# Performance work log

Measured on AMD Instinct MI355X. Metric: run time of the kernel, lower is better.

The kernel has to match this reference:

```python
import jax, jax.numpy as jnp
import numpy as np


def _patch_desc(x, patch_size):
    # x: (n, c, h, w). Replicate-pad by patch_size//2 and gather all
    # patch_size*patch_size shifted views -> (n, c*p*p, h*w) descriptors.
    n, c, h, w = x.shape
    step = patch_size // 2
    y = jnp.pad(x, ((0, 0), (0, 0), (step, step), (step, step)), mode='edge')
    feats = [y[:, :, i:i + h, j:j + w]
             for i in range(patch_size) for j in range(patch_size)]
    d = jnp.stack(feats, axis=2)            # (n, c, p*p, h, w)
    return d.reshape(n, c * patch_size * patch_size, h * w)


def setup_inputs() -> dict:
    key = jax.random.key(0)
    k1, k2 = jax.random.split(key)
    n, c, h, w = 4, 16, 64, 64
    s = jax.random.normal(k1, (n, c, h, w), dtype=jnp.float32)
    t = jax.random.normal(k2, (n, c, h, w), dtype=jnp.float32)
    return {"s": s, "t": t, "patch_size": 3}


def reference(s, t, patch_size):
    n, c, h, w = s.shape
    q = _patch_desc(s, patch_size)          # (n, d, hw) source queries
    p = _patch_desc(t, patch_size)          # (n, d, hw) target points
    # Squared-L2 nearest neighbor per source patch (exact version of FLANN kNN)
    qn = jnp.sum(q * q, axis=1)             # (n, hw)
    pn = jnp.sum(p * p, axis=1)             # (n, hw)
    cross = jnp.einsum('ndi,ndj->nij', q, p)  # (n, hw_q, hw_t)
    d2 = qn[:, :, None] - 2.0 * cross + pn[:, None, :]
    idx = jnp.argmin(d2, axis=2)            # (n, hw) flat target index
    nnd = jnp.min(d2, axis=2)               # (n, hw) squared distance
    idy = idx // w
    idx_x = idx % w
    nnf = jnp.stack([idy.reshape(n, h, w), idx_x.reshape(n, h, w)], axis=1)
    nnd = nnd.reshape(n, 1, h, w)
    return nnf.astype(jnp.int32), nnd
```

## Files before the change

### kernel.cpp

```cpp
#include <hip/hip_runtime.h>


#define N_  4
#define C_  16
#define H_  64
#define W_  64
#define HW_ 4096
#define K_  160
#define SPLITS_M 4
#define KKSTRIDE 528

#define SPLITS_V 4
#define TILES_PER_SPLIT_V 4

typedef _Float16 f16;
typedef _Float16 f16x8 __attribute__((ext_vector_type(8)));
typedef float    f32x4 __attribute__((ext_vector_type(4)));

__device__ __forceinline__ int iclamp(int v, int lo, int hi) {
    return v < lo ? lo : (v > hi ? hi : v);
}

__device__ __forceinline__ void async_ld16(const void* g, void* l) {
    __builtin_amdgcn_global_load_lds(
        (const __attribute__((address_space(1))) unsigned int*)g,
        (__attribute__((address_space(3))) unsigned int*)l, 16, 0, 0);
}

__global__ __launch_bounds__(256)
void build_desc_norms_kernel(const float* __restrict__ s,
                             const float* __restrict__ t,
                             f16* __restrict__ Qh, f16* __restrict__ Ql,
                             f16* __restrict__ Ph, f16* __restrict__ Pl,
                             float* __restrict__ pn,
                             float* __restrict__ qn) {
    const int y0  = blockIdx.x;
    const int n   = blockIdx.y;
    const int src = blockIdx.z;
    const float* img = (src ? s : t) + n * (C_ * HW_);
    f16* Dh = src ? Qh : Ph;
    f16* Dl = src ? Ql : Pl;
    float* nrm = src ? qn : pn;

    __shared__ float imgS[3][C_][W_];
    __shared__ float nS[4][W_];
    const int tid = threadIdx.x;
    #pragma unroll
    for (int k = 0; k < 12; ++k) {
        const int idx = tid + k * 256;
        const int x = idx & 63, c = (idx >> 6) & 15, r = idx >> 10;
        const int gy = iclamp(y0 + r - 1, 0, H_ - 1);
        imgS[r][c][x] = img[c * HW_ + gy * W_ + x];
    }
    __syncthreads();

    const int q = tid >> 6, x = tid & 63;
    const int pix = y0 * W_ + x;
    float nacc = 0.f;
    #pragma unroll
    for (int u = 0; u < 5; ++u) {
        const int kk = q * 5 + u;
        f16x8 hv, lv;
        if (kk < 18) {
            const int d  = kk >> 1;
            const int c0 = (kk & 1) * 8;
            const int dy = (d * 11) >> 5;
            const int dx = d - dy * 3;
            const int xs = iclamp(x + dx - 1, 0, W_ - 1);
            #pragma unroll
            for (int cc = 0; cc < 8; ++cc) {
                const float v = imgS[dy][c0 + cc][xs];
                const f16 h = (f16)v;
                hv[cc] = h;
                lv[cc] = (f16)(v - (float)h);
                nacc += v * v;
            }
        } else {
            #pragma unroll
            for (int cc = 0; cc < 8; ++cc) { hv[cc] = (f16)0.f; lv[cc] = (f16)0.f; }
        }
        const size_t off = ((size_t)(n * 20 + kk) * HW_ + pix) * 8;
        *(f16x8*)&Dh[off] = hv;
        *(f16x8*)&Dl[off] = lv;
    }
    nS[q][x] = nacc;
    __syncthreads();
    if (tid < W_)
        nrm[n * HW_ + pix] = nS[0][tid] + nS[1][tid] + nS[2][tid] + nS[3][tid];
}

__global__ __launch_bounds__(256)
void mfma_nn_kernel(const f16* __restrict__ Qh, const f16* __restrict__ Ql,
                    const f16* __restrict__ Ph, const f16* __restrict__ Pl,
                    const float* __restrict__ pn_g,
                    unsigned long long* __restrict__ partial) {
    const int bid   = blockIdx.x;
    const int split = bid & 3;
    const int n     = (bid >> 2) & 3;
    const int iblk  = bid >> 4;
    const int tid  = threadIdx.x;
    const int wave = tid >> 6, lane = tid & 63;
    const int m = lane & 15, quad = lane >> 4;
    const int irow0 = iblk * 128 + wave * 32;

    __shared__ f16 B0[20 * KKSTRIDE];
    __shared__ f16 B1[20 * KKSTRIDE];
    __shared__ f16 B2[20 * KKSTRIDE];
    __shared__ float pnS[1024];

    f16x8 Ah[2][5], Al[2][5];
    #pragma unroll
    for (int is = 0; is < 2; ++is)
        #pragma unroll
        for (int kc = 0; kc < 5; ++kc) {
            const size_t off = ((size_t)(n * 20 + kc * 4 + quad) * HW_ +
                                irow0 + is * 16 + m) * 8;
            Ah[is][kc] = *(const f16x8*)(Qh + off);
            Al[is][kc] = *(const f16x8*)(Ql + off);
        }

    const int jsplit0 = split * 1024;
    #pragma unroll
    for (int k = 0; k < 4; ++k)
        pnS[tid + k * 256] = pn_g[n * HW_ + jsplit0 + tid + k * 256];

    float    bd[2][4];
    unsigned bj[2][4];
    #pragma unroll
    for (int is = 0; is < 2; ++is)
        #pragma unroll
        for (int rg = 0; rg < 4; ++rg) { bd[is][rg] = 3.0e38f; bj[is][rg] = 0u; }

    const int skk  = wave * 5;
    const int sarr = lane >> 5;
    const int srow = lane & 31;
    const f16* sbase = sarr ? Pl : Ph;

    #define STAGE(BUF, T)                                                     \
        {   _Pragma("unroll")                                                 \
            for (int u = 0; u < 5; ++u) {                                     \
                const int kk = skk + u;                                       \
                const f16* g = sbase + ((size_t)(n * 20 + kk) * HW_ +         \
                                        jsplit0 + (T) * 32 + srow) * 8;       \
                async_ld16(g, (void*)&BUF[kk * KKSTRIDE + lane * 8]);         \
            }                                                                 \
        }

    #define COMPUTE(BUF, T)                                                   \
        {   _Pragma("unroll")                                                 \
            for (int js = 0; js < 2; ++js) {                                  \
                f32x4 Cf[2];                                                  \
                Cf[0] = (f32x4){0.f, 0.f, 0.f, 0.f};                          \
                Cf[1] = (f32x4){0.f, 0.f, 0.f, 0.f};                          \
                _Pragma("unroll")                                             \
                for (int kc = 0; kc < 5; ++kc) {                              \
                    const int kb = (kc * 4 + quad) * KKSTRIDE +               \
                                   (js * 16 + m) * 8;                         \
                    const f16x8 bh = *(const f16x8*)&BUF[kb];                 \
                    const f16x8 bl = *(const f16x8*)&BUF[kb + 256];           \
                    _Pragma("unroll")                                         \
                    for (int is = 0; is < 2; ++is) {                          \
                        Cf[is] = __builtin_amdgcn_mfma_f32_16x16x32_f16(      \
                            Ah[is][kc], bh, Cf[is], 0, 0, 0);                 \
                        Cf[is] = __builtin_amdgcn_mfma_f32_16x16x32_f16(      \
                            Al[is][kc], bh, Cf[is], 0, 0, 0);                 \
                        Cf[is] = __builtin_amdgcn_mfma_f32_16x16x32_f16(      \
                            Ah[is][kc], bl, Cf[is], 0, 0, 0);                 \
                    }                                                         \
                }                                                             \
                const int jloc = (T) * 32 + js * 16 + m;                      \
                const float pnv = pnS[jloc];                                  \
                _Pragma("unroll")                                             \
                for (int is = 0; is < 2; ++is)                                \
                    _Pragma("unroll")                                         \
                    for (int rg = 0; rg < 4; ++rg) {                          \
                        const float d = fmaf(Cf[is][rg], -2.f, pnv);          \
                        if (d < bd[is][rg]) {                                 \
                            bd[is][rg] = d;                                   \
                            bj[is][rg] = (unsigned)jloc;                      \
                        }                                                     \
                    }                                                         \
            }                                                                 \
        }

    STAGE(B0, 0)
    STAGE(B1, 1)
    __syncthreads();

    for (int g = 0; g < 10; ++g) {
        const int t = g * 3;
        asm volatile("s_waitcnt vmcnt(5)" ::: "memory");
        asm volatile("s_barrier" ::: "memory");
        STAGE(B2, t + 2)
        COMPUTE(B0, t)
        asm volatile("s_waitcnt vmcnt(5)" ::: "memory");
        asm volatile("s_barrier" ::: "memory");
        STAGE(B0, t + 3)
        COMPUTE(B1, t + 1)
        asm volatile("s_waitcnt vmcnt(5)" ::: "memory");
        asm volatile("s_barrier" ::: "memory");
        STAGE(B1, t + 4)
        COMPUTE(B2, t + 2)
    }
    asm volatile("s_waitcnt vmcnt(5)" ::: "memory");
    asm volatile("s_barrier" ::: "memory");
    COMPUTE(B0, 30)
    asm volatile("s_waitcnt vmcnt(0)" ::: "memory");
    asm volatile("s_barrier" ::: "memory");
    COMPUTE(B1, 31)
    #undef STAGE
    #undef COMPUTE

    #pragma unroll
    for (int is = 0; is < 2; ++is)
        #pragma unroll
        for (int rg = 0; rg < 4; ++rg) {
            float    d = bd[is][rg];
            unsigned j = (unsigned)jsplit0 + bj[is][rg];
            #pragma unroll
            for (int off = 1; off < 16; off <<= 1) {
                const float    od = __shfl_xor(d, off, 64);
                const unsigned oj = __shfl_xor(j, off, 64);
                const bool take = (od < d) || (od == d && oj < j);
                d = take ? od : d;
                j = take ? oj : j;
            }
            if (m == 0) {
                const int i = irow0 + is * 16 + quad * 4 + rg;
                partial[(size_t)(split * N_ + n) * HW_ + i] =
                    ((unsigned long long)j << 32) |
                    (unsigned long long)__float_as_uint(d);
            }
        }
}

__global__ __launch_bounds__(256)
void finalize_mfma_kernel(const unsigned long long* __restrict__ partial,
                          const float* __restrict__ qn_g,
                          float* __restrict__ out) {
    const int id  = blockIdx.x * 256 + threadIdx.x;
    const int n   = id >> 12;
    const int pix = id & 4095;
    float    bd = 3.0e38f;
    unsigned bj = 0u;
    #pragma unroll
    for (int sp = 0; sp < SPLITS_M; ++sp) {
        const unsigned long long v = partial[(size_t)(sp * N_ + n) * HW_ + pix];
        const float    d = __uint_as_float((unsigned)(v & 0xffffffffull));
        const unsigned j = (unsigned)(v >> 32);
        const bool take = (d < bd) || (d == bd && j < bj);
        bd = take ? d : bd;
        bj = take ? j : bj;
    }
    out[n * 2 * HW_ + pix]            = (float)(bj >> 6);
    out[n * 2 * HW_ + HW_ + pix]      = (float)(bj & 63);
    out[N_ * 2 * HW_ + n * HW_ + pix] = bd + qn_g[n * HW_ + pix];
}

__global__ __launch_bounds__(256)
void prep_norms_kernel(const float* __restrict__ s,
                       const float* __restrict__ t,
                       float* __restrict__ pn,
                       float* __restrict__ qn) {
    const int gid   = blockIdx.x * 256 + threadIdx.x;
    const int which = gid >> 14;
    const int id    = gid & 16383;
    const int n     = id >> 12;
    const int pix   = id & 4095;
    const int y = pix >> 6, x = pix & 63;
    const float* base = (which ? s : t) + n * (C_ * HW_);
    float acc = 0.f;
    for (int c = 0; c < C_; ++c) {
        const float* bc = base + c * HW_;
        #pragma unroll
        for (int dy = 0; dy < 3; ++dy) {
            const float* br = bc + iclamp(y + dy - 1, 0, H_ - 1) * W_;
            #pragma unroll
            for (int dx = 0; dx < 3; ++dx) {
                float v = br[iclamp(x + dx - 1, 0, W_ - 1)];
                acc += v * v;
            }
        }
    }
    (which ? qn : pn)[id] = acc;
}

__global__ __launch_bounds__(256)
void patchmatch_main_kernel(const float* __restrict__ s,
                            const float* __restrict__ t,
                            const float* __restrict__ pn_g,
                            const float* __restrict__ qn_g,
                            unsigned long long* __restrict__ partial) {
    const int yq    = blockIdx.x;
    const int n     = blockIdx.y;
    const int split = blockIdx.z;
    const int tid  = threadIdx.x;
    const int tx   = tid & 15;
    const int ty   = tid >> 4;
    const int i0   = ty * 4;
    const int jrow = tx >> 2;
    const int jx0  = (tx & 3) * 16;

    __shared__ float qS[C_][3][68];
    __shared__ float tS[C_][6][68];
    __shared__ float qnS[W_];

    const float* sb = s + n * (C_ * HW_);
    const float* tb = t + n * (C_ * HW_);

    #pragma unroll
    for (int k = 0; k < 3; ++k) {
        const int id = tid + k * 256;
        const int sg = id & 15;
        const int c  = (id >> 4) & 15;
        const int r  = id >> 8;
        const int gr = iclamp(yq + r - 1, 0, H_ - 1);
        const float4 v = *(const float4*)&sb[c * HW_ + gr * W_ + sg * 4];
        float* dst = &qS[c][r][1 + sg * 4];
        dst[0] = v.x; dst[1] = v.y; dst[2] = v.z; dst[3] = v.w;
    }
    if (tid < 48) {
        const int c  = tid & 15;
        const int r  = tid >> 4;
        const int gr = iclamp(yq + r - 1, 0, H_ - 1);
        qS[c][r][0]  = sb[c * HW_ + gr * W_];
        qS[c][r][65] = sb[c * HW_ + gr * W_ + 63];
    }
    if (tid < W_) qnS[tid] = qn_g[n * HW_ + yq * W_ + tid];

    unsigned long long best[4] = {~0ull, ~0ull, ~0ull, ~0ull};

    for (int ytl = 0; ytl < TILES_PER_SPLIT_V; ++ytl) {
        const int yt = split * TILES_PER_SPLIT_V + ytl;
        __syncthreads();
        #pragma unroll
        for (int k = 0; k < 6; ++k) {
            const int id = tid + k * 256;
            const int sg = id & 15;
            const int c  = (id >> 4) & 15;
            const int r  = id >> 8;
            const int gr = iclamp(4 * yt + r - 1, 0, H_ - 1);
            const float4 v = *(const float4*)&tb[c * HW_ + gr * W_ + sg * 4];
            float* dst = &tS[c][r][1 + sg * 4];
            dst[0] = v.x; dst[1] = v.y; dst[2] = v.z; dst[3] = v.w;
        }
        if (tid < 96) {
            const int c  = tid & 15;
            const int r  = tid >> 4;
            const int gr = iclamp(4 * yt + r - 1, 0, H_ - 1);
            tS[c][r][0]  = tb[c * HW_ + gr * W_];
            tS[c][r][65] = tb[c * HW_ + gr * W_ + 63];
        }
        __syncthreads();

        float acc[4][16];
        #pragma unroll
        for (int a = 0; a < 4; ++a)
            #pragma unroll
            for (int b = 0; b < 16; ++b) acc[a][b] = 0.f;

        for (int c = 0; c < C_; ++c) {
            #pragma unroll
            for (int dy = 0; dy < 3; ++dy) {
                float qv[6], tv[18];
                *(float4*)&qv[0] = *(const float4*)&qS[c][dy][i0];
                *(float2*)&qv[4] = *(const float2*)&qS[c][dy][i0 + 4];
                const float* trow = &tS[c][jrow + dy][jx0];
                *(float4*)&tv[0]  = *(const float4*)&trow[0];
                *(float4*)&tv[4]  = *(const float4*)&trow[4];
                *(float4*)&tv[8]  = *(const float4*)&trow[8];
                *(float4*)&tv[12] = *(const float4*)&trow[12];
                *(float2*)&tv[16] = *(const float2*)&trow[16];
                #pragma unroll
                for (int dx = 0; dx < 3; ++dx)
                    #pragma unroll
                    for (int a = 0; a < 4; ++a)
                        #pragma unroll
                        for (int b = 0; b < 16; ++b)
                            acc[a][b] += qv[a + dx] * tv[b + dx];
            }
        }

        const int jbase = yt * 256 + jrow * W_ + jx0;
        float pnv[16];
        const float* png = &pn_g[n * HW_ + jbase];
        *(float4*)&pnv[0]  = *(const float4*)&png[0];
        *(float4*)&pnv[4]  = *(const float4*)&png[4];
        *(float4*)&pnv[8]  = *(const float4*)&png[8];
        *(float4*)&pnv[12] = *(const float4*)&png[12];
        #pragma unroll
        for (int a = 0; a < 4; ++a) {
            const float qn = qnS[i0 + a];
            #pragma unroll
            for (int b = 0; b < 16; ++b) {
                const float d2 = qn + pnv[b] - 2.f * acc[a][b];
                unsigned long long cand =
                    ((unsigned long long)__float_as_uint(d2) << 32) |
                    (unsigned)(jbase + b);
                best[a] = cand < best[a] ? cand : best[a];
            }
        }
    }

    #pragma unroll
    for (int a = 0; a < 4; ++a) {
        unsigned long long v = best[a];
        #pragma unroll
        for (int mm = 8; mm >= 1; mm >>= 1) {
            unsigned long long o = __shfl_xor(v, mm, 64);
            v = o < v ? o : v;
        }
        best[a] = v;
    }
    if (tx == 0) {
        #pragma unroll
        for (int a = 0; a < 4; ++a)
            partial[((split * N_ + n) * HW_) + yq * W_ + i0 + a] = best[a];
    }
}

__global__ __launch_bounds__(256)
void finalize_kernel(const unsigned long long* __restrict__ partial,
                     float* __restrict__ out) {
    const int id  = blockIdx.x * 256 + threadIdx.x;
    const int n   = id >> 12;
    const int pix = id & 4095;
    unsigned long long best = ~0ull;
    #pragma unroll
    for (int sp = 0; sp < SPLITS_V; ++sp) {
        unsigned long long v = partial[(sp * N_ + n) * HW_ + pix];
        best = v < best ? v : best;
    }
    const unsigned j = (unsigned)(best & 0xffffffffu);
    const float d2 = __uint_as_float((unsigned)(best >> 32));
    out[n * 2 * HW_ + pix]            = (float)(j >> 6);
    out[n * 2 * HW_ + HW_ + pix]      = (float)(j & 63);
    out[N_ * 2 * HW_ + n * HW_ + pix] = d2;
}

__global__ __launch_bounds__(256)
void patchmatch_mono_kernel(const float* __restrict__ s,
                            const float* __restrict__ t,
                            float* __restrict__ out) {
    const int yq  = blockIdx.x;
    const int n   = blockIdx.y;
    const int tid = threadIdx.x;
    const int tx  = tid & 15;
    const int ty  = tid >> 4;
    const int i0  = ty * 4;
    const int jrow = tx >> 3;
    const int jx0  = (tx & 7) * 8;

    __shared__ float qS[C_][3][68];
    __shared__ float tS[C_][4][68];
    __shared__ float pnS[HW_];
    __shared__ float qnS[W_];

    const float* sb = s + n * (C_ * HW_);
    const float* tb = t + n * (C_ * HW_);

    for (int jj = tid; jj < HW_; jj += 256) {
        const int y = jj >> 6, x = jj & 63;
        float acc = 0.f;
        for (int c = 0; c < C_; ++c) {
            const float* tc = tb + c * HW_;
            #pragma unroll
            for (int dy = 0; dy < 3; ++dy) {
                const float* tr = tc + iclamp(y + dy - 1, 0, H_ - 1) * W_;
                #pragma unroll
                for (int dx = 0; dx < 3; ++dx) {
                    float v = tr[iclamp(x + dx - 1, 0, W_ - 1)];
                    acc += v * v;
                }
            }
        }
        pnS[jj] = acc;
    }
    for (int idx = tid; idx < C_ * 3 * 66; idx += 256) {
        const int c   = idx / (3 * 66);
        const int rem = idx - c * (3 * 66);
        const int rr  = rem / 66;
        const int xi  = rem - rr * 66;
        qS[c][rr][xi] = sb[c * HW_ + iclamp(yq + rr - 1, 0, H_ - 1) * W_ +
                           iclamp(xi - 1, 0, W_ - 1)];
    }
    __syncthreads();
    if (tid < W_) {
        float acc = 0.f;
        for (int c = 0; c < C_; ++c)
            #pragma unroll
            for (int dy = 0; dy < 3; ++dy)
                #pragma unroll
                for (int dx = 0; dx < 3; ++dx) {
                    float v = qS[c][dy][tid + dx];
                    acc += v * v;
                }
        qnS[tid] = acc;
    }

    unsigned long long best[4] = {~0ull, ~0ull, ~0ull, ~0ull};
    for (int yt = 0; yt < 32; ++yt) {
        __syncthreads();
        for (int idx = tid; idx < C_ * 4 * 66; idx += 256) {
            const int c   = idx / (4 * 66);
            const int rem = idx - c * (4 * 66);
            const int rr  = rem / 66;
            const int xi  = rem - rr * 66;
            tS[c][rr][xi] = tb[c * HW_ + iclamp(2 * yt + rr - 1, 0, H_ - 1) * W_ +
                               iclamp(xi - 1, 0, W_ - 1)];
        }
        __syncthreads();

        float acc[4][8];
        #pragma unroll
        for (int a = 0; a < 4; ++a)
            #pragma unroll
            for (int b = 0; b < 8; ++b) acc[a][b] = 0.f;

        for (int c = 0; c < C_; ++c) {
            #pragma unroll
            for (int dy = 0; dy < 3; ++dy) {
                float qv[8], tv[12];
                *(float4*)&qv[0] = *(const float4*)&qS[c][dy][i0];
                *(float4*)&qv[4] = *(const float4*)&qS[c][dy][i0 + 4];
                const float* trow = &tS[c][jrow + dy][jx0];
                *(float4*)&tv[0] = *(const float4*)&trow[0];
                *(float4*)&tv[4] = *(const float4*)&trow[4];
                *(float4*)&tv[8] = *(const float4*)&trow[8];
                #pragma unroll
                for (int dx = 0; dx < 3; ++dx)
                    #pragma unroll
                    for (int a = 0; a < 4; ++a)
                        #pragma unroll
                        for (int b = 0; b < 8; ++b)
                            acc[a][b] += qv[a + dx] * tv[b + dx];
            }
        }
        const int rbase = (2 * yt + jrow) * W_ + jx0;
        #pragma unroll
        for (int a = 0; a < 4; ++a) {
            const float qn = qnS[i0 + a];
            #pragma unroll
            for (int b = 0; b < 8; ++b) {
                const int j = rbase + b;
                const float d2 = qn + pnS[j] - 2.f * acc[a][b];
                unsigned long long cand =
                    ((unsigned long long)__float_as_uint(d2) << 32) | (unsigned)j;
                best[a] = cand < best[a] ? cand : best[a];
            }
        }
    }
    #pragma unroll
    for (int a = 0; a < 4; ++a) {
        unsigned long long v = best[a];
        #pragma unroll
        for (int mm = 8; mm >= 1; mm >>= 1) {
            unsigned long long o = __shfl_xor(v, mm, 64);
            v = o < v ? o : v;
        }
        best[a] = v;
    }
    if (tx == 0) {
        #pragma unroll
        for (int a = 0; a < 4; ++a) {
            const int x = i0 + a;
            const unsigned j = (unsigned)(best[a] & 0xffffffffu);
            const float d2 = __uint_as_float((unsigned)(best[a] >> 32));
            const int pix = yq * W_ + x;
            out[n * 2 * HW_ + pix]            = (float)(j >> 6);
            out[n * 2 * HW_ + HW_ + pix]      = (float)(j & 63);
            out[N_ * 2 * HW_ + n * HW_ + pix] = d2;
        }
    }
}

extern "C" void kernel_launch(void* const* d_in, const int* in_sizes, int n_in,
                              void* d_out, int out_size, void* d_ws, size_t ws_size,
                              hipStream_t stream) {
    const float* s = (const float*)d_in[0];
    const float* t = (const float*)d_in[1];
    float* out = (float*)d_out;

    const size_t norm_b  = (size_t)N_ * HW_ * 4;
    const size_t part_b  = (size_t)SPLITS_M * N_ * HW_ * 8;
    const size_t desc_b  = (size_t)N_ * HW_ * K_ * 2;
    const size_t need_m  = 2 * norm_b + part_b + 4 * desc_b;

    if (ws_size >= need_m) {
        char* w = (char*)d_ws;
        float* pn = (float*)w;                       w += norm_b;
        float* qn = (float*)w;                       w += norm_b;
        unsigned long long* partial = (unsigned long long*)w; w += part_b;
        f16* Qh = (f16*)w;  w += desc_b;
        f16* Ql = (f16*)w;  w += desc_b;
        f16* Ph = (f16*)w;  w += desc_b;
        f16* Pl = (f16*)w;

        build_desc_norms_kernel<<<dim3(64, N_, 2), 256, 0, stream>>>(
            s, t, Qh, Ql, Ph, Pl, pn, qn);
        mfma_nn_kernel<<<512, 256, 0, stream>>>(Qh, Ql, Ph, Pl, pn, partial);
        finalize_mfma_kernel<<<64, 256, 0, stream>>>(partial, qn, out);
        return;
    }

    const size_t need_v = 2 * norm_b + (size_t)SPLITS_V * N_ * HW_ * 8;
    if (ws_size >= need_v) {
        float* pn = (float*)d_ws;
        float* qn = pn + N_ * HW_;
        unsigned long long* partial =
            (unsigned long long*)((char*)d_ws + 2 * norm_b);
        prep_norms_kernel<<<128, 256, 0, stream>>>(s, t, pn, qn);
        dim3 grid(H_, N_, SPLITS_V);
        patchmatch_main_kernel<<<grid, 256, 0, stream>>>(s, t, pn, qn, partial);
        finalize_kernel<<<64, 256, 0, stream>>>(partial, out);
        return;
    }

    dim3 grid(H_, N_);
    patchmatch_mono_kernel<<<grid, 256, 0, stream>>>(s, t, out);
}
```

Before: 126.0 us.

## Switch NN search to 32x32x16 MFMA, drop zero K padding, fold norm into accumulator

The MFMA nearest-neighbour kernel now uses 32x32x16 f16 MFMAs over the true 18 K-chunks instead of 16x16x32 MFMAs over 20 padded chunks. This cuts wasted MFMA work and LDS staging, and the descriptor builder no longer writes the zero padding. The accumulator is seeded with -0.5*pn so the argmin becomes an argmax of the raw accumulator, with the scale restored at the end. It also adds a two-blocks-per-CU launch bound, setprio around the MFMA sections, and uneven per-wave staging counts with matching waitcnts. The cost is a 16-element accumulator with 16 best-so-far pairs per lane, which raises register pressure, and a wider 32-lane reduction.

```diff
diff --git a/kernel.cpp b/kernel.cpp
--- a/kernel.cpp
+++ b/kernel.cpp
@@ -16,6 +16,7 @@
 typedef _Float16 f16;
 typedef _Float16 f16x8 __attribute__((ext_vector_type(8)));
 typedef float    f32x4 __attribute__((ext_vector_type(4)));
+typedef float    f32x16 __attribute__((ext_vector_type(16)));
 
 __device__ __forceinline__ int iclamp(int v, int lo, int hi) {
     return v < lo ? lo : (v > hi ? hi : v);
@@ -60,8 +61,8 @@
     #pragma unroll
     for (int u = 0; u < 5; ++u) {
         const int kk = q * 5 + u;
-        f16x8 hv, lv;
         if (kk < 18) {
+            f16x8 hv, lv;
             const int d  = kk >> 1;
             const int c0 = (kk & 1) * 8;
             const int dy = (d * 11) >> 5;
@@ -75,13 +76,10 @@
                 lv[cc] = (f16)(v - (float)h);
                 nacc += v * v;
             }
-        } else {
-            #pragma unroll
-            for (int cc = 0; cc < 8; ++cc) { hv[cc] = (f16)0.f; lv[cc] = (f16)0.f; }
-        }
-        const size_t off = ((size_t)(n * 20 + kk) * HW_ + pix) * 8;
-        *(f16x8*)&Dh[off] = hv;
-        *(f16x8*)&Dl[off] = lv;
+            const size_t off = ((size_t)(n * 20 + kk) * HW_ + pix) * 8;
+            *(f16x8*)&Dh[off] = hv;
+            *(f16x8*)&Dl[off] = lv;
+        }
     }
     nS[q][x] = nacc;
     __syncthreads();
@@ -89,7 +87,7 @@
         nrm[n * HW_ + pix] = nS[0][tid] + nS[1][tid] + nS[2][tid] + nS[3][tid];
 }
 
-__global__ __launch_bounds__(256)
+__global__ __launch_bounds__(256, 2)
 void mfma_nn_kernel(const f16* __restrict__ Qh, const f16* __restrict__ Ql,
                     const f16* __restrict__ Ph, const f16* __restrict__ Pl,
                     const float* __restrict__ pn_g,
@@ -100,87 +98,79 @@
     const int iblk  = bid >> 4;
     const int tid  = threadIdx.x;
     const int wave = tid >> 6, lane = tid & 63;
-    const int m = lane & 15, quad = lane >> 4;
+    const int col  = lane & 31;
+    const int half = lane >> 5;
     const int irow0 = iblk * 128 + wave * 32;
 
-    __shared__ f16 B0[20 * KKSTRIDE];
-    __shared__ f16 B1[20 * KKSTRIDE];
-    __shared__ f16 B2[20 * KKSTRIDE];
+    __shared__ f16 B0[18 * KKSTRIDE];
+    __shared__ f16 B1[18 * KKSTRIDE];
+    __shared__ f16 B2[18 * KKSTRIDE];
     __shared__ float pnS[1024];
 
-    f16x8 Ah[2][5], Al[2][5];
-    #pragma unroll
-    for (int is = 0; is < 2; ++is)
-        #pragma unroll
-        for (int kc = 0; kc < 5; ++kc) {
-            const size_t off = ((size_t)(n * 20 + kc * 4 + quad) * HW_ +
-                                irow0 + is * 16 + m) * 8;
-            Ah[is][kc] = *(const f16x8*)(Qh + off);
-            Al[is][kc] = *(const f16x8*)(Ql + off);
-        }
+    f16x8 Ah[9], Al[9];
+    #pragma unroll
+    for (int c = 0; c < 9; ++c) {
+        const size_t off = ((size_t)(n * 20 + 2 * c + half) * HW_ +
+                            irow0 + col) * 8;
+        Ah[c] = *(const f16x8*)(Qh + off);
+        Al[c] = *(const f16x8*)(Ql + off);
+    }
 
     const int jsplit0 = split * 1024;
     #pragma unroll
     for (int k = 0; k < 4; ++k)
         pnS[tid + k * 256] = pn_g[n * HW_ + jsplit0 + tid + k * 256];
 
-    float    bd[2][4];
-    unsigned bj[2][4];
-    #pragma unroll
-    for (int is = 0; is < 2; ++is)
-        #pragma unroll
-        for (int rg = 0; rg < 4; ++rg) { bd[is][rg] = 3.0e38f; bj[is][rg] = 0u; }
-
-    const int skk  = wave * 5;
-    const int sarr = lane >> 5;
-    const int srow = lane & 31;
-    const f16* sbase = sarr ? Pl : Ph;
+    float    bd[16];
+    unsigned bj[16];
+    #pragma unroll
+    for (int r = 0; r < 16; ++r) { bd[r] = -3.0e38f; bj[r] = 0u; }
+
+    const int nst = (wave < 2) ? 5 : 4;
+    const int kk0 = (wave < 2) ? wave * 5 : 10 + (wave - 2) * 4;
+    const f16* sbase = half ? Pl : Ph;
 
     #define STAGE(BUF, T)                                                     \
         {   _Pragma("unroll")                                                 \
             for (int u = 0; u < 5; ++u) {                                     \
-                const int kk = skk + u;                                       \
-                const f16* g = sbase + ((size_t)(n * 20 + kk) * HW_ +         \
-                                        jsplit0 + (T) * 32 + srow) * 8;       \
-                async_ld16(g, (void*)&BUF[kk * KKSTRIDE + lane * 8]);         \
+                if (u < nst) {                                                \
+                    const int kk = kk0 + u;                                   \
+                    const f16* g = sbase + ((size_t)(n * 20 + kk) * HW_ +     \
+                                            jsplit0 + (T) * 32 + col) * 8;    \
+                    async_ld16(g, (void*)&BUF[kk * KKSTRIDE + lane * 8]);     \
+                }                                                             \
             }                                                                 \
         }
 
+    #define TWAIT()                                                           \
+        {   if (wave < 2) asm volatile("s_waitcnt vmcnt(5)" ::: "memory");    \
+            else          asm volatile("s_waitcnt vmcnt(4)" ::: "memory");    \
+            asm volatile("s_barrier" ::: "memory");                           \
+        }
+
     #define COMPUTE(BUF, T)                                                   \
-        {   _Pragma("unroll")                                                 \
-            for (int js = 0; js < 2; ++js) {                                  \
-                f32x4 Cf[2];                                                  \
-                Cf[0] = (f32x4){0.f, 0.f, 0.f, 0.f};                          \
-                Cf[1] = (f32x4){0.f, 0.f, 0.f, 0.f};                          \
-                _Pragma("unroll")                                             \
-                for (int kc = 0; kc < 5; ++kc) {                              \
-                    const int kb = (kc * 4 + quad) * KKSTRIDE +               \
-                                   (js * 16 + m) * 8;                         \
-                    const f16x8 bh = *(const f16x8*)&BUF[kb];                 \
-                    const f16x8 bl = *(const f16x8*)&BUF[kb + 256];           \
-                    _Pragma("unroll")                                         \
-                    for (int is = 0; is < 2; ++is) {                          \
-                        Cf[is] = __builtin_amdgcn_mfma_f32_16x16x32_f16(      \
-                            Ah[is][kc], bh, Cf[is], 0, 0, 0);                 \
-                        Cf[is] = __builtin_amdgcn_mfma_f32_16x16x32_f16(      \
-                            Al[is][kc], bh, Cf[is], 0, 0, 0);                 \
-                        Cf[is] = __builtin_amdgcn_mfma_f32_16x16x32_f16(      \
-                            Ah[is][kc], bl, Cf[is], 0, 0, 0);                 \
-                    }                                                         \
-                }                                                             \
-                const int jloc = (T) * 32 + js * 16 + m;                      \
-                const float pnv = pnS[jloc];                                  \
-                _Pragma("unroll")                                             \
-                for (int is = 0; is < 2; ++is)                                \
-                    _Pragma("unroll")                                         \
-                    for (int rg = 0; rg < 4; ++rg) {                          \
-                        const float d = fmaf(Cf[is][rg], -2.f, pnv);          \
-                        if (d < bd[is][rg]) {                                 \
-                            bd[is][rg] = d;                                   \
-                            bj[is][rg] = (unsigned)jloc;                      \
-                        }                                                     \
-                    }                                                         \
+        {   const float pnv = -0.5f * pnS[(T) * 32 + col];                    \
+            f32x16 Cf;                                                        \
+            _Pragma("unroll")                                                 \
+            for (int r = 0; r < 16; ++r) Cf[r] = pnv;                         \
+            __builtin_amdgcn_s_setprio(1);                                    \
+            _Pragma("unroll")                                                 \
+            for (int c = 0; c < 9; ++c) {                                     \
+                const int kb = (2 * c + half) * KKSTRIDE + col * 8;           \
+                const f16x8 bh = *(const f16x8*)&BUF[kb];                     \
+                const f16x8 bl = *(const f16x8*)&BUF[kb + 256];               \
+                Cf = __builtin_amdgcn_mfma_f32_32x32x16_f16(                  \
+                    Ah[c], bh, Cf, 0, 0, 0);                                  \
+                Cf = __builtin_amdgcn_mfma_f32_32x32x16_f16(                  \
+                    Al[c], bh, Cf, 0, 0, 0);                                  \
+                Cf = __builtin_amdgcn_mfma_f32_32x32x16_f16(                  \
+                    Ah[c], bl, Cf, 0, 0, 0);                                  \
             }                                                                 \
+            __builtin_amdgcn_s_setprio(0);                                    \
+            const unsigned jloc = (unsigned)((T) * 32 + col);                 \
+            _Pragma("unroll")                                                 \
+            for (int r = 0; r < 16; ++r)                                      \
+                if (Cf[r] > bd[r]) { bd[r] = Cf[r]; bj[r] = jloc; }           \
         }
 
     STAGE(B0, 0)
@@ -189,49 +179,44 @@
 
     for (int g = 0; g < 10; ++g) {
         const int t = g * 3;
-        asm volatile("s_waitcnt vmcnt(5)" ::: "memory");
-        asm volatile("s_barrier" ::: "memory");
+        TWAIT()
         STAGE(B2, t + 2)
         COMPUTE(B0, t)
-        asm volatile("s_waitcnt vmcnt(5)" ::: "memory");
-        asm volatile("s_barrier" ::: "memory");
+        TWAIT()
         STAGE(B0, t + 3)
         COMPUTE(B1, t + 1)
-        asm volatile("s_waitcnt vmcnt(5)" ::: "memory");
-        asm volatile("s_barrier" ::: "memory");
+        TWAIT()
         STAGE(B1, t + 4)
         COMPUTE(B2, t + 2)
     }
-    asm volatile("s_waitcnt vmcnt(5)" ::: "memory");
-    asm volatile("s_barrier" ::: "memory");
+    TWAIT()
     COMPUTE(B0, 30)
     asm volatile("s_waitcnt vmcnt(0)" ::: "memory");
     asm volatile("s_barrier" ::: "memory");
     COMPUTE(B1, 31)
     #undef STAGE
+    #undef TWAIT
     #undef COMPUTE
 
     #pragma unroll
-    for (int is = 0; is < 2; ++is)
-        #pragma unroll
-        for (int rg = 0; rg < 4; ++rg) {
-            float    d = bd[is][rg];
-            unsigned j = (unsigned)jsplit0 + bj[is][rg];
-            #pragma unroll
-            for (int off = 1; off < 16; off <<= 1) {
-                const float    od = __shfl_xor(d, off, 64);
-                const unsigned oj = __shfl_xor(j, off, 64);
-                const bool take = (od < d) || (od == d && oj < j);
-                d = take ? od : d;
-                j = take ? oj : j;
-            }
-            if (m == 0) {
-                const int i = irow0 + is * 16 + quad * 4 + rg;
-                partial[(size_t)(split * N_ + n) * HW_ + i] =
-                    ((unsigned long long)j << 32) |
-                    (unsigned long long)__float_as_uint(d);
-            }
-        }
+    for (int r = 0; r < 16; ++r) {
+        float    d = bd[r];
+        unsigned j = (unsigned)jsplit0 + bj[r];
+        #pragma unroll
+        for (int off = 1; off < 32; off <<= 1) {
+            const float    od = __shfl_xor(d, off, 64);
+            const unsigned oj = __shfl_xor(j, off, 64);
+            const bool take = (od > d) || (od == d && oj < j);
+            d = take ? od : d;
+            j = take ? oj : j;
+        }
+        if (col == 0) {
+            const int i = irow0 + (r & 3) + 8 * (r >> 2) + 4 * half;
+            partial[(size_t)(split * N_ + n) * HW_ + i] =
+                ((unsigned long long)j << 32) |
+                (unsigned long long)__float_as_uint(-2.f * d);
+        }
+    }
 }
 
 __global__ __launch_bounds__(256)
```

Result: no change. 125.1 us (-0.7%).
